# Kernel tuning notes

Hardware: AMD Instinct MI355X
Metric: run time of the kernel (lower is better)

## Reference

```python
import jax, jax.numpy as jnp
import numpy as np

N = 50000   # nodes
E = 800000  # edges (avg degree 16)
DIMS = [16, 256, 128, 64, 32, 4]  # in_feats -> hidden stack -> num_classes


def setup_inputs() -> dict:
    key = jax.random.key(0)
    ks = jax.random.split(key, 16)
    src = jax.random.randint(ks[0], (E,), 0, N, dtype=jnp.int32)
    dst = jax.random.randint(ks[1], (E,), 0, N, dtype=jnp.int32)
    x = jax.random.normal(ks[2], (N, DIMS[0]), dtype=jnp.float32)
    efet = jax.random.uniform(ks[3], (E, 1), dtype=jnp.float32)
    inp = {"x": x, "efet": efet, "src": src, "dst": dst}
    for i in range(5):
        inp[f"W{i+1}"] = jax.random.normal(ks[4 + i], (DIMS[i], DIMS[i + 1]), dtype=jnp.float32) * 0.05
        inp[f"b{i+1}"] = jnp.zeros((DIMS[i + 1],), dtype=jnp.float32)
    return inp


def reference(x, efet, src, dst, W1, b1, W2, b2, W3, b3, W4, b4, W5, b5):
    ones = jnp.ones((E,), jnp.float32)
    out_deg = jax.ops.segment_sum(ones, src, num_segments=N)
    in_deg = jax.ops.segment_sum(ones, dst, num_segments=N)
    # DGL GraphConv norm='both': D_out^{-1/2} on src side, D_in^{-1/2} on dst side (deg clamped to 1)
    out_norm = (1.0 / jnp.sqrt(jnp.maximum(out_deg, 1.0)))[:, None]
    in_norm = (1.0 / jnp.sqrt(jnp.maximum(in_deg, 1.0)))[:, None]

    def graph_conv(h, W, b):
        m = (h * out_norm) @ W               # [N, out]
        agg = jax.ops.segment_sum(m[src], dst, num_segments=N)
        return agg * in_norm + b

    def edge_weighted_agg(h):
        # update_all(u_mul_e('h','efet','m'), sum('m','h'))
        return jax.ops.segment_sum(h[src] * efet, dst, num_segments=N)

    h1 = jax.nn.relu(edge_weighted_agg(jax.nn.relu(graph_conv(x, W1, b1))))
    h2 = jax.nn.relu(edge_weighted_agg(jax.nn.relu(graph_conv(h1, W2, b2))))
    h3 = jax.nn.relu(edge_weighted_agg(jax.nn.relu(graph_conv(h2, W3, b3))))
    h4 = jax.nn.relu(graph_conv(h3, W4, b4))
    h5 = graph_conv(h4, W5, b5)
    return h5
```

## Files before the change

kernel.cpp:

```cpp
#include <hip/hip_runtime.h>
#include <hip/hip_fp16.h>

#define BLOCK 256
#define PAD 16
#define SCAP 4096
#define OVCAP 4096
#define BUFCAP 4352

#define NBIN 416
#define CAPBIG 16
#define BINA_THREADS 1024
#define BINA_BLOCKS 256

typedef _Float16 h2v __attribute__((ext_vector_type(2)));

#if defined(__has_builtin) && __has_builtin(__builtin_amdgcn_sched_barrier)
#define SCHED_FENCE() __builtin_amdgcn_sched_barrier(0)
#else
#define SCHED_FENCE()
#endif

__device__ inline void st4f(__half* p, float4 v) {
    __half2 a = __floats2half2_rn(v.x, v.y);
    __half2 b = __floats2half2_rn(v.z, v.w);
    uint2 u;
    u.x = *reinterpret_cast<unsigned*>(&a);
    u.y = *reinterpret_cast<unsigned*>(&b);
    *(uint2*)p = u;
}
__device__ inline void st4f(float* p, float4 v) { *(float4*)p = v; }
__device__ inline void st8f(float* p, const float f[8]) {
    *(float4*)p       = make_float4(f[0], f[1], f[2], f[3]);
    *(float4*)(p + 4) = make_float4(f[4], f[5], f[6], f[7]);
}
__device__ inline void st8f(__half* p, const float f[8]) {
    union { __half2 h[4]; float4 v; } u;
    u.h[0] = __floats2half2_rn(f[0], f[1]);
    u.h[1] = __floats2half2_rn(f[2], f[3]);
    u.h[2] = __floats2half2_rn(f[4], f[5]);
    u.h[3] = __floats2half2_rn(f[6], f[7]);
    *(float4*)p = u.v;
}
__device__ inline void ld2v(const __half* p, float* f) {
    float2 v = __half22float2(*(const __half2*)p); f[0] = v.x; f[1] = v.y;
}
__device__ inline void ld4v(const __half* p, float* f) {
    float2 r = *(const float2*)p;
    const __half2* h = (const __half2*)&r;
    float2 a = __half22float2(h[0]), b = __half22float2(h[1]);
    f[0] = a.x; f[1] = a.y; f[2] = b.x; f[3] = b.y;
}
__device__ inline void ld8v(const __half* p, float* f) {
    float4 r = *(const float4*)p;
    const __half2* h = (const __half2*)&r;
#pragma unroll
    for (int j = 0; j < 4; ++j) {
        float2 fj = __half22float2(h[j]);
        f[2*j] = fj.x; f[2*j+1] = fj.y;
    }
}
__device__ inline float4 ld4f(const float* p) { return *(const float4*)p; }
__device__ inline float edgeW(int2 er) {
    return __half2float(__ushort_as_half((unsigned short)(er.y & 0xffff)));
}
__device__ inline h2v packh2(float a, float b) {
    h2v r; r.x = (_Float16)a; r.y = (_Float16)b; return r;
}
__device__ inline int2 ntld2(const int2* p) {
    long long v = __builtin_nontemporal_load((const long long*)p);
    union { long long l; int2 i; } u; u.l = v; return u.i;
}

__global__ __launch_bounds__(BINA_THREADS) void binA_kernel(
    const int* __restrict__ src, const int* __restrict__ dst,
    const float* __restrict__ efet,
    int* __restrict__ degO_x,
    int* __restrict__ scur, int* __restrict__ ovcur,
    int2* __restrict__ staging, int2* __restrict__ overflow,
    int N, int E, int NBUK) {
    __shared__ int2 bins[NBIN][CAPBIG];
    __shared__ int  lcnt[NBIN];
    const int t = threadIdx.x;
    for (int b = t; b < NBIN; b += BINA_THREADS) lcnt[b] = 0;
    __syncthreads();

    const int nbuk_c = (NBUK < NBIN) ? NBUK : NBIN;
    const int chunk = (E + gridDim.x - 1) / gridDim.x;
    const int e0 = blockIdx.x * chunk;
    int e1 = e0 + chunk; if (e1 > E) e1 = E;
    const int xcc = __builtin_amdgcn_s_getreg(63508) & 7;

    for (int base = e0; base < e1; base += BINA_THREADS) {
        const int e = base + t;
        if (e < e1) {
            int s = __builtin_nontemporal_load(src + e);
            int d = __builtin_nontemporal_load(dst + e);
            float w = __builtin_nontemporal_load(efet + e);
            atomicAdd(&degO_x[(size_t)xcc * N + s], 1);
            int b = d >> 7;
            int2 rec;
            rec.x = s;
            rec.y = (int)__half_as_ushort(__float2half(w)) | ((d & 127) << 16);
            int pos = (b < NBIN) ? atomicAdd(&lcnt[b], 1) : CAPBIG;
            if (pos < CAPBIG) {
                bins[b][pos] = rec;
            } else {
                int q = atomicAdd(&ovcur[b * PAD], 1);
                if (q < OVCAP) overflow[(size_t)b * OVCAP + q] = rec;
            }
        }
        __syncthreads();
        for (int b = t; b < nbuk_c; b += BINA_THREADS) {
            int c = lcnt[b];
            if (c > CAPBIG) c = CAPBIG;
            int nf = c & ~7;
            if (nf) {
                int g = atomicAdd(&scur[b * PAD], nf);
                if (g + nf <= SCAP) {
                    const int4* s4 = (const int4*)&bins[b][0];
                    int4* d4 = (int4*)(staging + (size_t)b * SCAP + g);
                    for (int i = 0; i < (nf >> 1); ++i) d4[i] = s4[i];
                } else {
                    for (int i = 0; i < nf; ++i) {
                        int gg = g + i;
                        if (gg < SCAP) staging[(size_t)b * SCAP + gg] = bins[b][i];
                        else {
                            int q = atomicAdd(&ovcur[b * PAD], 1);
                            if (q < OVCAP) overflow[(size_t)b * OVCAP + q] = bins[b][i];
                        }
                    }
                }
                int rem = c - nf;
                for (int i = 0; i < rem; ++i) bins[b][i] = bins[b][nf + i];
                lcnt[b] = rem;
            }
        }
        __syncthreads();
    }
    for (int b = t; b < nbuk_c; b += BINA_THREADS) {
        int c = lcnt[b];
        if (c > CAPBIG) c = CAPBIG;
        if (c > 0) {
            int q = atomicAdd(&ovcur[b * PAD], c);
            for (int i = 0; i < c; ++i)
                if (q + i < OVCAP) overflow[(size_t)b * OVCAP + q + i] = bins[b][i];
        }
    }
}

__global__ __launch_bounds__(256) void binB_kernel(
    const int* __restrict__ scur, const int* __restrict__ ovcur,
    const int2* __restrict__ staging, const int2* __restrict__ overflow,
    int* __restrict__ gcur, int2* __restrict__ rowSpan, float* __restrict__ normI,
    int2* __restrict__ edges,
    const int* __restrict__ degO_x, const float* __restrict__ x,
    __half* __restrict__ xh, float* __restrict__ normO, int N) {
    __shared__ int2 buf[BUFCAP];
    __shared__ int cnt[128];
    __shared__ int rs[128];
    __shared__ int cur[128];
    __shared__ float nO[128];
    __shared__ int base;
    int b = blockIdx.x;
    int v0 = b << 7;
    int t = threadIdx.x;
    int nn = N - v0; if (nn > 128) nn = 128;
    if (t < 128) cnt[t] = 0;

    int c = scur[b * PAD];
    if (c > SCAP) c = SCAP;
    int oc = ovcur[b * PAD];
    if (oc > OVCAP) oc = OVCAP;
    int total = c + oc;
    if (total > BUFCAP) total = BUFCAP;
    __syncthreads();

    {
        const int2* reg = staging + (size_t)b * SCAP;
        for (int i = t; i < c; i += 256) {
            if (i < BUFCAP) buf[i] = ntld2(reg + i);
        }
    }
    {
        const int2* reg = overflow + (size_t)b * OVCAP;
        for (int i = t; i < oc; i += 256) {
            int o = c + i;
            if (o < BUFCAP) buf[o] = ntld2(reg + i);
        }
    }
    __syncthreads();

    for (int i = t; i < total; i += 256)
        atomicAdd(&cnt[(buf[i].y >> 16) & 127], 1);
    __syncthreads();

    if (t == 0) {
        base = atomicAdd(gcur, total);
        int a2 = 0;
        for (int k = 0; k < 128; ++k) { rs[k] = a2; a2 += cnt[k]; }
    }
    __syncthreads();

    if (t < 128) {
        cur[t] = 0;
        int v = v0 + t;
        if (v < N) {
            int2 sp;
            sp.x = base + rs[t];
            sp.y = sp.x + cnt[t];
            rowSpan[v] = sp;
            normI[v] = rsqrtf(fmaxf((float)cnt[t], 1.0f));
            int dsum = 0;
#pragma unroll
            for (int k = 0; k < 8; ++k) dsum += degO_x[(size_t)k * N + v];
            float wv = rsqrtf(fmaxf((float)dsum, 1.0f));
            nO[t] = wv;
            normO[v] = wv;
        }
    }
    __syncthreads();

    for (int i = t; i < total; i += 256) {
        int2 rec = buf[i];
        int dl = (rec.y >> 16) & 127;
        int lp = atomicAdd(&cur[dl], 1);
        edges[base + rs[dl] + lp] = rec;
    }

    for (int i = t; i < nn * 4; i += 256) {
        int vl = i >> 2, cc = (i & 3) * 4;
        int v = v0 + vl;
        float4 f = ld4f(x + (size_t)v * 16 + cc);
        float wv = nO[vl];
        f.x *= wv; f.y *= wv; f.z *= wv; f.w *= wv;
        st4f(xh + (size_t)v * 16 + cc, f);
    }
}

template <int D>
__global__ __launch_bounds__(256) void agg8_kernel(
    const __half* __restrict__ in, __half* __restrict__ out,
    const int2* __restrict__ rowSpan, const int2* __restrict__ edges,
    int useW,
    const float* __restrict__ dstScale,
    const float* __restrict__ bias,
    int N, int relu) {
    constexpr int TPN = D / 8;
    constexpr int NN  = 256 / TPN;
    constexpr int ECAP = (NN * 32 < 2560) ? NN * 32 : 2560;
    __shared__ int2 eb[ECAP];
    __shared__ int s_w[2];
    const int t = threadIdx.x;
    const int v0 = blockIdx.x * NN;
    if (t == 0) {
        int vl = v0 + NN - 1; if (vl >= N) vl = N - 1;
        s_w[0] = rowSpan[v0].x;
        s_w[1] = rowSpan[vl].y;
    }
    __syncthreads();
    const int wbeg = s_w[0];
    int nst = s_w[1] - wbeg; if (nst > ECAP) nst = ECAP;
    for (int i = t; i < nst; i += 256) eb[i] = ntld2(&edges[wbeg + i]);
    __syncthreads();

    int v = v0 + t / TPN;
    int c8 = (t % TPN) * 8;
    if (v >= N) return;
    int2 sp = rowSpan[v];
    int beg = sp.x, end = sp.y;
    float a[8];
#pragma unroll
    for (int k = 0; k < 8; ++k) a[k] = 0.f;
    const __half* base = in + c8;

    auto erec = [&](int j) -> int2 {
        int o = j - wbeg;
        return (o < nst) ? eb[o] : edges[j];
    };

    int j = beg;
    for (; j + 8 <= end; j += 8) {
        int2 er[8];
#pragma unroll
        for (int q = 0; q < 8; ++q) er[q] = erec(j + q);
        SCHED_FENCE();
        float4 raw[8];
#pragma unroll
        for (int q = 0; q < 8; ++q) raw[q] = *(const float4*)(base + (size_t)er[q].x * D);
        SCHED_FENCE();
#pragma unroll
        for (int q = 0; q < 8; ++q) {
            float w = useW ? edgeW(er[q]) : 1.f;
            const __half2* h = (const __half2*)&raw[q];
#pragma unroll
            for (int p = 0; p < 4; ++p) {
                float2 fj = __half22float2(h[p]);
                a[2*p]   += fj.x * w;
                a[2*p+1] += fj.y * w;
            }
        }
    }
    if (j + 4 <= end) {
        int2 er[4];
#pragma unroll
        for (int q = 0; q < 4; ++q) er[q] = erec(j + q);
        SCHED_FENCE();
        float4 raw[4];
#pragma unroll
        for (int q = 0; q < 4; ++q) raw[q] = *(const float4*)(base + (size_t)er[q].x * D);
        SCHED_FENCE();
#pragma unroll
        for (int q = 0; q < 4; ++q) {
            float w = useW ? edgeW(er[q]) : 1.f;
            const __half2* h = (const __half2*)&raw[q];
#pragma unroll
            for (int p = 0; p < 4; ++p) {
                float2 fj = __half22float2(h[p]);
                a[2*p]   += fj.x * w;
                a[2*p+1] += fj.y * w;
            }
        }
        j += 4;
    }
    for (; j < end; ++j) {
        int2 er = erec(j);
        float w = useW ? edgeW(er) : 1.f;
        float xv[8];
        ld8v(base + (size_t)er.x * D, xv);
#pragma unroll
        for (int k = 0; k < 8; ++k) a[k] += xv[k] * w;
    }
    if (dstScale) {
        float sc = dstScale[v];
        if (bias) {
#pragma unroll
            for (int k = 0; k < 8; ++k) a[k] = a[k] * sc + bias[c8 + k];
        } else {
#pragma unroll
            for (int k = 0; k < 8; ++k) a[k] *= sc;
        }
    }
    if (relu) {
#pragma unroll
        for (int k = 0; k < 8; ++k) a[k] = fmaxf(a[k], 0.f);
    }
    st8f(out + (size_t)v * D + c8, a);
}

__global__ __launch_bounds__(256) void gc32_fused(
    const __half* __restrict__ in, float* __restrict__ t5,
    const int2* __restrict__ rowSpan, const int2* __restrict__ edges,
    const float* __restrict__ normI, const float* __restrict__ b4,
    const float* __restrict__ normO, const float* __restrict__ W5,
    int N) {
    constexpr int NN = 64;
    constexpr int ECAP = 2048;
    __shared__ int2 eb[ECAP];
    __shared__ int s_w[2];
    const int t = threadIdx.x;
    const int v0 = blockIdx.x * NN;
    if (t == 0) {
        int vl = v0 + NN - 1; if (vl >= N) vl = N - 1;
        s_w[0] = rowSpan[v0].x;
        s_w[1] = rowSpan[vl].y;
    }
    __syncthreads();
    const int wbeg = s_w[0];
    int nst = s_w[1] - wbeg; if (nst > ECAP) nst = ECAP;
    for (int i = t; i < nst; i += 256) eb[i] = ntld2(&edges[wbeg + i]);
    __syncthreads();

    int v = v0 + (t >> 2);
    int q = t & 3;
    int c8 = q * 8;
    if (v >= N) return;
    int2 sp = rowSpan[v];
    int beg = sp.x, end = sp.y;
    float a[8];
#pragma unroll
    for (int k = 0; k < 8; ++k) a[k] = 0.f;
    const __half* base = in + c8;

    auto erec = [&](int j) -> int2 {
        int o = j - wbeg;
        return (o < nst) ? eb[o] : edges[j];
    };

    int j = beg;
    for (; j + 8 <= end; j += 8) {
        int2 er[8];
#pragma unroll
        for (int p = 0; p < 8; ++p) er[p] = erec(j + p);
        SCHED_FENCE();
        float4 raw[8];
#pragma unroll
        for (int p = 0; p < 8; ++p) raw[p] = *(const float4*)(base + (size_t)er[p].x * 32);
        SCHED_FENCE();
#pragma unroll
        for (int p = 0; p < 8; ++p) {
            const __half2* h = (const __half2*)&raw[p];
#pragma unroll
            for (int s = 0; s < 4; ++s) {
                float2 fj = __half22float2(h[s]);
                a[2*s]   += fj.x;
                a[2*s+1] += fj.y;
            }
        }
    }
    for (; j < end; ++j) {
        int2 er = erec(j);
        float xv[8];
        ld8v(base + (size_t)er.x * 32, xv);
#pragma unroll
        for (int k = 0; k < 8; ++k) a[k] += xv[k];
    }
    float sc = normI[v];
#pragma unroll
    for (int k = 0; k < 8; ++k) a[k] = fmaxf(a[k] * sc + b4[c8 + k], 0.f);

    float p4[4] = {0.f, 0.f, 0.f, 0.f};
#pragma unroll
    for (int k = 0; k < 8; ++k) {
        float4 wr = ld4f(W5 + (size_t)(c8 + k) * 4);
        p4[0] += a[k] * wr.x; p4[1] += a[k] * wr.y;
        p4[2] += a[k] * wr.z; p4[3] += a[k] * wr.w;
    }
#pragma unroll
    for (int c = 0; c < 4; ++c) {
        p4[c] += __shfl_xor(p4[c], 1);
        p4[c] += __shfl_xor(p4[c], 2);
    }
    if (q == 0) {
        float no = normO[v];
        st4f(t5 + (size_t)v * 4, make_float4(p4[0]*no, p4[1]*no, p4[2]*no, p4[3]*no));
    }
}

__global__ void agg4_kernel(const float* __restrict__ in, float* __restrict__ out,
                            const int2* __restrict__ rowSpan, const int2* __restrict__ edges,
                            const float* __restrict__ dstScale, const float* __restrict__ bias,
                            int N) {
    int v = blockIdx.x * blockDim.x + threadIdx.x;
    if (v >= N) return;
    int2 sp = rowSpan[v];
    int beg = sp.x, end = sp.y;
    float ax = 0.f, ay = 0.f, az = 0.f, aw = 0.f;
    int j = beg;
    for (; j + 4 <= end; j += 4) {
        int2 er[4];
#pragma unroll
        for (int q = 0; q < 4; ++q) er[q] = edges[j + q];
        SCHED_FENCE();
        float4 raw[4];
#pragma unroll
        for (int q = 0; q < 4; ++q) raw[q] = ld4f(in + (size_t)er[q].x * 4);
        SCHED_FENCE();
#pragma unroll
        for (int q = 0; q < 4; ++q) {
            ax += raw[q].x; ay += raw[q].y; az += raw[q].z; aw += raw[q].w;
        }
    }
    for (; j < end; ++j) {
        float4 val = ld4f(in + (size_t)edges[j].x * 4);
        ax += val.x; ay += val.y; az += val.z; aw += val.w;
    }
    float sc = dstScale[v];
    ax = ax * sc + bias[0];
    ay = ay * sc + bias[1];
    az = az * sc + bias[2];
    aw = aw * sc + bias[3];
    st4f(out + (size_t)v * 4, make_float4(ax, ay, az, aw));
}

template <int KT, int RPT, int TN>
__global__ __launch_bounds__(256) void gemm_tiled(
    const __half* __restrict__ A, const float* __restrict__ W,
    const float* __restrict__ rowScaleIn,
    const float* __restrict__ rowScaleOut,
    const float* __restrict__ bias,
    __half* __restrict__ C, int N, int K1, int relu)
{
    constexpr int NC8 = TN / 8;
    constexpr int RT  = 256 / NC8;
    constexpr int TM  = RT * RPT;
    constexpr int AFPT = TM * KT / 256;
    constexpr int KP  = KT / 2;
    constexpr int WRS = TN + (TN >> 5) * 4;
    static_assert(AFPT == 2 || AFPT == 4 || AFPT == 8 || AFPT == 16, "unexpected AFPT");
    static_assert(RPT == 1 || RPT == 2 || RPT == 4 || RPT == 8, "unexpected RPT");

    __shared__ h2v Alds[KP][TM];
    __shared__ h2v Wlds[KP][WRS];

    const int t    = threadIdx.x;
    const int cg   = t % NC8;
    const int rt   = t / NC8;
    const int c0   = cg * 8;
    const int row0 = blockIdx.x * TM;
    const int pc0  = c0 + ((c0 >> 5) << 2);

    const int arow   = t % TM;
    const int akb    = (t / TM) * AFPT;
    const int arow_g = row0 + arow;
    float rsc = 1.0f;
    if (rowScaleIn && arow_g < N) rsc = rowScaleIn[arow_g];

    float acc[RPT][8];
#pragma unroll
    for (int r = 0; r < RPT; ++r)
#pragma unroll
        for (int j = 0; j < 8; ++j) acc[r][j] = 0.f;

    for (int k0 = 0; k0 < K1; k0 += KT) {
        float av[AFPT];
        if (arow_g < N) {
            const __half* ag = A + (size_t)arow_g * K1 + k0 + akb;
            if constexpr (AFPT == 16) { ld8v(ag, av); ld8v(ag + 8, av + 8); }
            else if constexpr (AFPT == 8) ld8v(ag, av);
            else if constexpr (AFPT == 4) ld4v(ag, av);
            else                          ld2v(ag, av);
        } else {
#pragma unroll
            for (int j = 0; j < AFPT; ++j) av[j] = 0.f;
        }
#pragma unroll
        for (int j = 0; j < AFPT; j += 2)
            Alds[(akb + j) >> 1][arow] = packh2(av[j] * rsc, av[j + 1] * rsc);

        for (int i = t; i < KP * TN; i += 256) {
            int kp = i / TN, c = i % TN;
            Wlds[kp][c + ((c >> 5) << 2)] = packh2(W[(size_t)(k0 + 2 * kp) * TN + c],
                                                   W[(size_t)(k0 + 2 * kp + 1) * TN + c]);
        }
        __syncthreads();

#pragma unroll
        for (int kp = 0; kp < KP; ++kp) {
            h2v a2[RPT];
            if constexpr (RPT == 8) {
                union { float4 f; h2v h[4]; } u0, u1;
                u0.f = *(const float4*)&Alds[kp][rt * 8];
                u1.f = *(const float4*)&Alds[kp][rt * 8 + 4];
                a2[0] = u0.h[0]; a2[1] = u0.h[1]; a2[2] = u0.h[2]; a2[3] = u0.h[3];
                a2[4] = u1.h[0]; a2[5] = u1.h[1]; a2[6] = u1.h[2]; a2[7] = u1.h[3];
            } else if constexpr (RPT == 4) {
                union { float4 f; h2v h[4]; } u;
                u.f = *(const float4*)&Alds[kp][rt * 4];
                a2[0] = u.h[0]; a2[1] = u.h[1]; a2[2] = u.h[2]; a2[3] = u.h[3];
            } else if constexpr (RPT == 2) {
                union { float2 f; h2v h[2]; } u;
                u.f = *(const float2*)&Alds[kp][rt * 2];
                a2[0] = u.h[0]; a2[1] = u.h[1];
            } else {
                a2[0] = Alds[kp][rt];
            }
            union { float4 f; h2v h[4]; } w0, w1;
            w0.f = *(const float4*)&Wlds[kp][pc0];
            w1.f = *(const float4*)&Wlds[kp][pc0 + 4];
#pragma unroll
            for (int r = 0; r < RPT; ++r) {
                acc[r][0] = __builtin_amdgcn_fdot2(a2[r], w0.h[0], acc[r][0], false);
                acc[r][1] = __builtin_amdgcn_fdot2(a2[r], w0.h[1], acc[r][1], false);
                acc[r][2] = __builtin_amdgcn_fdot2(a2[r], w0.h[2], acc[r][2], false);
                acc[r][3] = __builtin_amdgcn_fdot2(a2[r], w0.h[3], acc[r][3], false);
                acc[r][4] = __builtin_amdgcn_fdot2(a2[r], w1.h[0], acc[r][4], false);
                acc[r][5] = __builtin_amdgcn_fdot2(a2[r], w1.h[1], acc[r][5], false);
                acc[r][6] = __builtin_amdgcn_fdot2(a2[r], w1.h[2], acc[r][6], false);
                acc[r][7] = __builtin_amdgcn_fdot2(a2[r], w1.h[3], acc[r][7], false);
            }
        }
        __syncthreads();
    }

#pragma unroll
    for (int r = 0; r < RPT; ++r) {
        int row_g = row0 + rt * RPT + r;
        if (row_g >= N) continue;
        float f[8];
        if (rowScaleOut) {
            float sc = rowScaleOut[row_g];
#pragma unroll
            for (int j = 0; j < 8; ++j) f[j] = acc[r][j] * sc + bias[c0 + j];
        } else {
#pragma unroll
            for (int j = 0; j < 8; ++j) f[j] = acc[r][j];
        }
        if (relu) {
#pragma unroll
            for (int j = 0; j < 8; ++j) f[j] = fmaxf(f[j], 0.f);
        }
        st8f(C + (size_t)row_g * TN + c0, f);
    }
}

static inline int nblk(long n) { return (int)((n + BLOCK - 1) / BLOCK); }

extern "C" void kernel_launch(void* const* d_in, const int* in_sizes, int n_in,
                              void* d_out, int out_size, void* d_ws, size_t ws_size,
                              hipStream_t stream) {
    const float* x    = (const float*)d_in[0];
    const float* efet = (const float*)d_in[1];
    const int*   src  = (const int*)d_in[2];
    const int*   dst  = (const int*)d_in[3];
    const float* W1 = (const float*)d_in[4];  const float* b1 = (const float*)d_in[5];
    const float* W2 = (const float*)d_in[6];  const float* b2 = (const float*)d_in[7];
    const float* W3 = (const float*)d_in[8];  const float* b3 = (const float*)d_in[9];
    const float* W4 = (const float*)d_in[10]; const float* b4 = (const float*)d_in[11];
    const float* W5 = (const float*)d_in[12]; const float* b5 = (const float*)d_in[13];
    float* out = (float*)d_out;

    const int N = in_sizes[0] / 16;
    const int E = in_sizes[2];
    const int NBUK = (N + 127) / 128;

    float* fws = (float*)d_ws;
    size_t o = 0;
    auto alloc = [&](size_t nf) { float* p = fws + o; o += (nf + 3) & ~(size_t)3; return p; };
    float*  normO     = alloc(N);
    float*  normI     = alloc(N);
    int2*   rowSpan   = (int2*)alloc(2 * (size_t)N);
    int2*   edges     = (int2*)alloc(2 * (size_t)E);
    int*    degO_x    = (int*)alloc(8 * (size_t)N);
    int*    scur      = (int*)alloc((size_t)NBUK * PAD);
    int*    ovcur     = (int*)alloc((size_t)NBUK * PAD);
    int*    gcur      = (int*)alloc(4);
    size_t zeroBytes  = (8 * (size_t)N + (size_t)NBUK * PAD + (size_t)NBUK * PAD + 4) * 4;
    int2*   staging   = (int2*)alloc(2 * (size_t)NBUK * SCAP);
    int2*   overflow  = (int2*)alloc(2 * (size_t)NBUK * OVCAP);
    __half* xh        = (__half*)alloc(8 * (size_t)N);
    __half* bufA      = (__half*)alloc(128 * (size_t)N);
    __half* bufB      = (__half*)alloc(128 * (size_t)N);
    __half* bufC      = (__half*)alloc(64 * (size_t)N);
    float*  t5f       = (float*)bufB;

    (void)hipMemsetAsync(degO_x, 0, zeroBytes, stream);
    binA_kernel<<<BINA_BLOCKS, BINA_THREADS, 0, stream>>>(
        src, dst, efet, degO_x, scur, ovcur, staging, overflow, N, E, NBUK);
    binB_kernel<<<NBUK, 256, 0, stream>>>(scur, ovcur, staging, overflow,
                                          gcur, rowSpan, normI, edges,
                                          degO_x, x, xh, normO, N);

    agg8_kernel<16><<<nblk((long)N * 2), BLOCK, 0, stream>>>(
        xh, bufC, rowSpan, edges, 0, nullptr, nullptr, N, 0);
    gemm_tiled<16, 8, 256><<<(N + 63) / 64, 256, 0, stream>>>(
        bufC, W1, nullptr, normI, b1, bufA, N, 16, 1);

    gemm_tiled<32, 8, 128><<<(N + 127) / 128, 256, 0, stream>>>(
        bufA, W2, nullptr, nullptr, nullptr, bufB, N, 256, 0);
    agg8_kernel<128><<<nblk((long)N * 16), BLOCK, 0, stream>>>(
        bufB, bufC, rowSpan, edges, 1, normO, nullptr, N, 0);
    agg8_kernel<128><<<nblk((long)N * 16), BLOCK, 0, stream>>>(
        bufC, bufB, rowSpan, edges, 0, normI, b2, N, 1);

    gemm_tiled<32, 4, 64><<<(N + 127) / 128, 256, 0, stream>>>(
        bufB, W3, nullptr, nullptr, nullptr, bufA, N, 128, 0);
    agg8_kernel<64><<<nblk((long)N * 8), BLOCK, 0, stream>>>(
        bufA, bufC, rowSpan, edges, 1, normO, nullptr, N, 0);
    agg8_kernel<64><<<nblk((long)N * 8), BLOCK, 0, stream>>>(
        bufC, bufB, rowSpan, edges, 0, normI, b3, N, 1);

    gemm_tiled<32, 2, 32><<<(N + 127) / 128, 256, 0, stream>>>(
        bufB, W4, nullptr, nullptr, nullptr, bufA, N, 64, 0);
    agg8_kernel<32><<<nblk((long)N * 4), BLOCK, 0, stream>>>(
        bufA, bufC, rowSpan, edges, 1, normO, nullptr, N, 0);
    gc32_fused<<<nblk((long)N * 4), BLOCK, 0, stream>>>(
        bufC, t5f, rowSpan, edges, normI, b4, normO, W5, N);

    agg4_kernel<<<nblk((long)N), BLOCK, 0, stream>>>(
        t5f, out, rowSpan, edges, normI, b5, N);
}
```

Before: 404.9 us.

## Use MFMA matrix cores for hidden-layer GEMMs and retile first GEMM

Adds a gemm_mfma kernel that uses the 16x16x32 fp16 MFMA instruction with LDS-staged A and W fragments. It replaces the fdot2-based tiled GEMM for layers 2-4, and the first GEMM drops to 4 rows per thread with twice as many blocks. The aim is to move dense matmul work onto matrix cores and cut VALU time. W is still reloaded and converted from fp32 on every K step, and outputs are written as scalar halves, so those writes may not coalesce well.

```diff
diff --git a/kernel.cpp b/kernel.cpp
--- a/kernel.cpp
+++ b/kernel.cpp
@@ -13,6 +13,8 @@
 #define BINA_BLOCKS 256
 
 typedef _Float16 h2v __attribute__((ext_vector_type(2)));
+typedef _Float16 h8v __attribute__((ext_vector_type(8)));
+typedef float f4v __attribute__((ext_vector_type(4)));
 
 #if defined(__has_builtin) && __has_builtin(__builtin_amdgcn_sched_barrier)
 #define SCHED_FENCE() __builtin_amdgcn_sched_barrier(0)
@@ -472,6 +474,72 @@
     st4f(out + (size_t)v * 4, make_float4(ax, ay, az, aw));
 }
 
+template <int TN, int K1>
+__global__ __launch_bounds__(256) void gemm_mfma(
+    const __half* __restrict__ A, const float* __restrict__ W,
+    __half* __restrict__ C, int N)
+{
+    constexpr int NCT = TN / 16;
+    constexpr int NKS = K1 / 32;
+    __shared__ _Float16 Alds[4][64][8];
+    __shared__ _Float16 Blds[NCT][64][8];
+
+    const int t    = threadIdx.x;
+    const int w    = t >> 6;
+    const int lane = t & 63;
+    const int row0 = blockIdx.x * 64;
+
+    f4v acc[NCT];
+#pragma unroll
+    for (int ct = 0; ct < NCT; ++ct)
+#pragma unroll
+        for (int r = 0; r < 4; ++r) acc[ct][r] = 0.f;
+
+    const int srow   = t >> 2;
+    const int sq     = t & 3;
+    const int grow_s = row0 + srow;
+
+    for (int ks = 0; ks < NKS; ++ks) {
+        const int k0 = ks * 32;
+        {
+            h8v av;
+#pragma unroll
+            for (int jj = 0; jj < 8; ++jj) av[jj] = (_Float16)0;
+            if (grow_s < N)
+                av = *(const h8v*)(A + (size_t)grow_s * K1 + k0 + sq * 8);
+            *(h8v*)&Alds[srow >> 4][(sq << 4) | (srow & 15)][0] = av;
+        }
+        for (int idx = t; idx < 16 * TN; idx += 256) {
+            int k2 = idx / TN;
+            int c  = idx % TN;
+            int k  = k2 << 1;
+            h2v hv = packh2(W[(size_t)(k0 + k) * TN + c],
+                            W[(size_t)(k0 + k + 1) * TN + c]);
+            *(h2v*)&Blds[c >> 4][((k >> 3) << 4) | (c & 15)][k & 7] = hv;
+        }
+        __syncthreads();
+        h8v af = *(const h8v*)&Alds[w][lane][0];
+#pragma unroll
+        for (int ct = 0; ct < NCT; ++ct) {
+            h8v bf = *(const h8v*)&Blds[ct][lane][0];
+            acc[ct] = __builtin_amdgcn_mfma_f32_16x16x32_f16(af, bf, acc[ct], 0, 0, 0);
+        }
+        __syncthreads();
+    }
+
+    const int lr = (lane >> 4) << 2;
+    const int lc = lane & 15;
+#pragma unroll
+    for (int ct = 0; ct < NCT; ++ct) {
+#pragma unroll
+        for (int r = 0; r < 4; ++r) {
+            int grow = row0 + (w << 4) + lr + r;
+            if (grow < N)
+                C[(size_t)grow * TN + ct * 16 + lc] = __float2half(acc[ct][r]);
+        }
+    }
+}
+
 template <int KT, int RPT, int TN>
 __global__ __launch_bounds__(256) void gemm_tiled(
     const __half* __restrict__ A, const float* __restrict__ W,
@@ -487,7 +555,6 @@
     constexpr int KP  = KT / 2;
     constexpr int WRS = TN + (TN >> 5) * 4;
     static_assert(AFPT == 2 || AFPT == 4 || AFPT == 8 || AFPT == 16, "unexpected AFPT");
-    static_assert(RPT == 1 || RPT == 2 || RPT == 4 || RPT == 8, "unexpected RPT");
 
     __shared__ h2v Alds[KP][TM];
     __shared__ h2v Wlds[KP][WRS];
@@ -537,13 +604,7 @@
 #pragma unroll
         for (int kp = 0; kp < KP; ++kp) {
             h2v a2[RPT];
-            if constexpr (RPT == 8) {
-                union { float4 f; h2v h[4]; } u0, u1;
-                u0.f = *(const float4*)&Alds[kp][rt * 8];
-                u1.f = *(const float4*)&Alds[kp][rt * 8 + 4];
-                a2[0] = u0.h[0]; a2[1] = u0.h[1]; a2[2] = u0.h[2]; a2[3] = u0.h[3];
-                a2[4] = u1.h[0]; a2[5] = u1.h[1]; a2[6] = u1.h[2]; a2[7] = u1.h[3];
-            } else if constexpr (RPT == 4) {
+            if constexpr (RPT == 4) {
                 union { float4 f; h2v h[4]; } u;
                 u.f = *(const float4*)&Alds[kp][rt * 4];
                 a2[0] = u.h[0]; a2[1] = u.h[1]; a2[2] = u.h[2]; a2[3] = u.h[3];
@@ -612,6 +673,7 @@
     const int N = in_sizes[0] / 16;
     const int E = in_sizes[2];
     const int NBUK = (N + 127) / 128;
+    const int NB64 = (N + 63) / 64;
 
     float* fws = (float*)d_ws;
     size_t o = 0;
@@ -642,25 +704,22 @@
 
     agg8_kernel<16><<<nblk((long)N * 2), BLOCK, 0, stream>>>(
         xh, bufC, rowSpan, edges, 0, nullptr, nullptr, N, 0);
-    gemm_tiled<16, 8, 256><<<(N + 63) / 64, 256, 0, stream>>>(
+    gemm_tiled<16, 4, 256><<<(N + 31) / 32, 256, 0, stream>>>(
         bufC, W1, nullptr, normI, b1, bufA, N, 16, 1);
 
-    gemm_tiled<32, 8, 128><<<(N + 127) / 128, 256, 0, stream>>>(
-        bufA, W2, nullptr, nullptr, nullptr, bufB, N, 256, 0);
+    gemm_mfma<128, 256><<<NB64, 256, 0, stream>>>(bufA, W2, bufB, N);
     agg8_kernel<128><<<nblk((long)N * 16), BLOCK, 0, stream>>>(
         bufB, bufC, rowSpan, edges, 1, normO, nullptr, N, 0);
     agg8_kernel<128><<<nblk((long)N * 16), BLOCK, 0, stream>>>(
         bufC, bufB, rowSpan, edges, 0, normI, b2, N, 1);
 
-    gemm_tiled<32, 4, 64><<<(N + 127) / 128, 256, 0, stream>>>(
-        bufB, W3, nullptr, nullptr, nullptr, bufA, N, 128, 0);
+    gemm_mfma<64, 128><<<NB64, 256, 0, stream>>>(bufB, W3, bufA, N);
     agg8_kernel<64><<<nblk((long)N * 8), BLOCK, 0, stream>>>(
         bufA, bufC, rowSpan, edges, 1, normO, nullptr, N, 0);
     agg8_kernel<64><<<nblk((long)N * 8), BLOCK, 0, stream>>>(
         bufC, bufB, rowSpan, edges, 0, normI, b3, N, 1);
 
-    gemm_tiled<32, 2, 32><<<(N + 127) / 128, 256, 0, stream>>>(
-        bufB, W4, nullptr, nullptr, nullptr, bufA, N, 64, 0);
+    gemm_mfma<32, 64><<<NB64, 256, 0, stream>>>(bufB, W4, bufA, N);
     agg8_kernel<32><<<nblk((long)N * 4), BLOCK, 0, stream>>>(
         bufA, bufC, rowSpan, edges, 1, normO, nullptr, N, 0);
     gc32_fused<<<nblk((long)N * 4), BLOCK, 0, stream>>>(
```

Measured after the change: 373.2 us. 7.8% less time.
